# Kernel optimization log

Measured on AMD Instinct MI355X. Metric: run time of the kernel, lower is better.

The kernel has to match this reference:

```python
import jax, jax.numpy as jnp
import numpy as np

NUM_ROUTING = 3
EPS = 1e-8


def squash(s, axis):
    # s * (||s||^2 / (1 + ||s||^2)) / ||s||  along `axis`
    sq = jnp.sum(s * s, axis=axis, keepdims=True)
    return s * (sq / (1.0 + sq)) / jnp.sqrt(sq + EPS)


def setup_inputs() -> dict:
    key = jax.random.key(0)
    k1, k2 = jax.random.split(key)
    B, R, C, OUT, IN = 32, 2048, 32, 32, 16
    x = jax.random.normal(k1, (B, R, IN), dtype=jnp.float32)
    vote = jax.random.normal(k2, (R, C, OUT, IN), dtype=jnp.float32)
    return {"x": x, "vote": vote}


def reference(x, vote):
    # votes[b,r,c,o] = sum_i vote[r,c,o,i] * x[b,r,i]
    votes = jnp.einsum('rcoi,bri->brco', vote, x)  # [B,R,C,OUT]
    agreement = jnp.zeros_like(votes)
    verdict = None
    for _ in range(NUM_ROUTING):
        chairman = jax.nn.softmax(agreement, axis=1)          # softmax over routes
        summary = jnp.sum(chairman * votes, axis=1, keepdims=True)  # [B,1,C,OUT]
        verdict = squash(summary, axis=3)                     # squash over out_dim
        agreement = agreement + jnp.sum(votes * verdict, axis=3, keepdims=True)
    return verdict[:, 0, :, :]  # [B, C, OUT]
```

## Files before the change

### kernel.cpp

```cpp
#include <hip/hip_runtime.h>
#include <hip/hip_fp16.h>

#define B 32
#define R 2048
#define C 32
#define O 32
#define IN 16

typedef _Float16 hf2 __attribute__((ext_vector_type(2)));


__global__ __launch_bounds__(512, 4) void votes_kernel(
    const float* __restrict__ x,
    const float* __restrict__ vote,
    __half* __restrict__ votes_h)
{
  const int t = threadIdx.x;
  const int c = blockIdx.y * 2 + (t >> 8);
  const int tt = t & 255;
  const int rp_l = tt >> 4;
  const int op = tt & 15;
  const int r0 = blockIdx.x * 32;
  const int r = r0 + 2 * rp_l;
  const int rpg = blockIdx.x * 16 + rp_l;

  __shared__ unsigned int x_lds[32 * 32 * 8];

#pragma unroll
  for (int k = 0; k < 8; ++k) {
    int j = t + k * 512;
    int bb = j >> 7;
    int rr = (j >> 2) & 31;
    int ic = j & 3;
    float4 v = *reinterpret_cast<const float4*>(
        x + ((size_t)bb * R + r0 + rr) * IN + ic * 4);
    __half2 h01 = __float22half2_rn(make_float2(v.x, v.y));
    __half2 h23 = __float22half2_rn(make_float2(v.z, v.w));
    int w = (bb * 32 + rr) * 8 + 2 * ic;
    x_lds[w] = __builtin_bit_cast(unsigned int, h01);
    x_lds[w + 1] = __builtin_bit_cast(unsigned int, h23);
  }

  unsigned int wh[4][8];
#pragma unroll
  for (int p = 0; p < 2; ++p) {
#pragma unroll
    for (int q = 0; q < 2; ++q) {
      const float4* vp = reinterpret_cast<const float4*>(
          vote + (((size_t)(r + p) * C + c) * O + 2 * op + q) * IN);
#pragma unroll
      for (int k = 0; k < 4; ++k) {
        float4 f = vp[k];
        __half2 a = __float22half2_rn(make_float2(f.x, f.y));
        __half2 d = __float22half2_rn(make_float2(f.z, f.w));
        wh[p * 2 + q][2 * k] = __builtin_bit_cast(unsigned int, a);
        wh[p * 2 + q][2 * k + 1] = __builtin_bit_cast(unsigned int, d);
      }
    }
  }
  __syncthreads();

  __half* ob = votes_h + (size_t)c * 65536 + (size_t)rpg * 64 + op * 4;

#pragma unroll 2
  for (int bb = 0; bb < 32; ++bb) {
    const uint4* xr = reinterpret_cast<const uint4*>(
        &x_lds[(bb * 32 + 2 * rp_l) * 8]);
    uint4 xa = xr[0], xb = xr[1];
    uint4 xc = xr[2], xd = xr[3];
    unsigned int x0[8] = {xa.x, xa.y, xa.z, xa.w, xb.x, xb.y, xb.z, xb.w};
    unsigned int x1[8] = {xc.x, xc.y, xc.z, xc.w, xd.x, xd.y, xd.z, xd.w};
    float a00 = 0.f, a01 = 0.f, a10 = 0.f, a11 = 0.f;
#pragma unroll
    for (int k = 0; k < 8; ++k) {
      hf2 xv0 = __builtin_bit_cast(hf2, x0[k]);
      hf2 xv1 = __builtin_bit_cast(hf2, x1[k]);
      a00 = __builtin_amdgcn_fdot2(__builtin_bit_cast(hf2, wh[0][k]), xv0, a00, false);
      a01 = __builtin_amdgcn_fdot2(__builtin_bit_cast(hf2, wh[1][k]), xv0, a01, false);
      a10 = __builtin_amdgcn_fdot2(__builtin_bit_cast(hf2, wh[2][k]), xv1, a10, false);
      a11 = __builtin_amdgcn_fdot2(__builtin_bit_cast(hf2, wh[3][k]), xv1, a11, false);
    }
    __half2 w0 = __float22half2_rn(make_float2(a00, a10));
    __half2 w1 = __float22half2_rn(make_float2(a01, a11));
    uint2 pk;
    pk.x = __builtin_bit_cast(unsigned int, w0);
    pk.y = __builtin_bit_cast(unsigned int, w1);
    *reinterpret_cast<uint2*>(ob + (size_t)bb * C * 65536) = pk;
  }
}

__global__ __launch_bounds__(1024, 4) void routing_kernel(
    const __half* __restrict__ votes_h,
    float* __restrict__ out)
{
  const int b = blockIdx.x >> 5;
  const int c = blockIdx.x & 31;
  const int t = threadIdx.x;
  const int lane = t & 63;
  const int wave = t >> 6;
  const int g = t >> 5;
  const int o = t & 31;

  __shared__ unsigned int vmix[1024 * 34];
  __shared__ float2 e2[1024];
  __shared__ float red[32][33];
  __shared__ float vdf[32];
  __shared__ float scal_z[16];

  const uint4* src = reinterpret_cast<const uint4*>(
      votes_h + ((size_t)b * C + c) * 65536);
#pragma unroll
  for (int k = 0; k < 8; ++k) {
    int j = t + k * 1024;
    uint4 v = src[j];
    int rp = j >> 3;
    int q = j & 7;
    unsigned int* dst = &vmix[rp * 34 + 4 * q];
    uint2 a; a.x = v.x; a.y = v.y;
    uint2 d; d.x = v.z; d.y = v.w;
    *reinterpret_cast<uint2*>(dst) = a;
    *reinterpret_cast<uint2*>(dst + 2) = d;
  }
  __syncthreads();

  float a0 = 0.0f, a1 = 0.0f;
  float Zinv = 1.0f / 2048.0f;

  for (int iter = 0; iter < 3; ++iter) {
    if (iter > 0) {
      float e0 = __expf(a0), e1 = __expf(a1);
      float z = e0 + e1;
#pragma unroll
      for (int mask = 32; mask; mask >>= 1) z += __shfl_xor(z, mask);
      if (lane == 0) scal_z[wave] = z;
      e2[t] = make_float2(e0, e1);
      __syncthreads();
      float Z = 0.0f;
#pragma unroll
      for (int w = 0; w < 16; ++w) Z += scal_z[w];
      Zinv = 1.0f / Z;
    }

    {
      float s = 0.0f;
      const unsigned int* vb = &vmix[(size_t)g * 32 * 34 + o];
      if (iter == 0) {
#pragma unroll
        for (int j = 0; j < 32; ++j) {
          __half2 vv = __builtin_bit_cast(__half2, vb[j * 34]);
          s += __low2float(vv) + __high2float(vv);
        }
      } else {
        const float2* eb = &e2[g * 32];
#pragma unroll
        for (int j = 0; j < 32; ++j) {
          __half2 vv = __builtin_bit_cast(__half2, vb[j * 34]);
          float2 ee = eb[j];
          s += ee.x * __low2float(vv) + ee.y * __high2float(vv);
        }
      }
      red[o][g] = s;
    }
    __syncthreads();

    if (t < 32) {
      float S = 0.0f;
#pragma unroll
      for (int gg = 0; gg < 32; ++gg) S += red[t][gg];
      float summary = S * Zinv;
      float sq = summary * summary;
#pragma unroll
      for (int mask = 16; mask; mask >>= 1) sq += __shfl_xor(sq, mask);
      float scale = sq / ((1.0f + sq) * sqrtf(sq + 1e-8f));
      float vd = summary * scale;
      vdf[t] = vd;
      if (iter == 2) out[((size_t)b * C + c) * O + t] = vd;
    }
    __syncthreads();

    if (iter < 2) {
      float u0 = 0.0f, u1 = 0.0f;
      const unsigned int* vb = &vmix[(size_t)t * 34];
#pragma unroll
      for (int q = 0; q < 16; ++q) {
        uint2 vv = *reinterpret_cast<const uint2*>(vb + 2 * q);
        __half2 va = __builtin_bit_cast(__half2, vv.x);
        __half2 vbh = __builtin_bit_cast(__half2, vv.y);
        float vda = vdf[2 * q], vdb = vdf[2 * q + 1];
        u0 += __low2float(va) * vda + __low2float(vbh) * vdb;
        u1 += __high2float(va) * vda + __high2float(vbh) * vdb;
      }
      a0 += u0;
      a1 += u1;
    }
  }
}

extern "C" void kernel_launch(void* const* d_in, const int* in_sizes, int n_in,
                              void* d_out, int out_size, void* d_ws, size_t ws_size,
                              hipStream_t stream) {
  const float* x = (const float*)d_in[0];
  const float* vote = (const float*)d_in[1];
  float* out = (float*)d_out;
  __half* votes_h = (__half*)d_ws;

  votes_kernel<<<dim3(R / 32, C / 2), 512, 0, stream>>>(x, vote, votes_h);
  routing_kernel<<<dim3(B * C), 1024, 0, stream>>>(votes_h, out);
}
```

Before: 284.0 us.

## Split votes kernel over batch quarters and fuse first routing sum into load

The votes kernel now gives each block a single capsule c and 16 routes, with threads split across four batch quarters. This shrinks the shared x tile and raises the occupancy hint at the cost of reloading vote weights for more blocks. The routing kernel computes the iteration-0 uniform sum while staging votes into shared memory, using shuffle reductions, so the first strided shared-memory pass is skipped. An extra barrier is added at the end of each routing iteration.

```diff
diff --git a/kernel.cpp b/kernel.cpp
--- a/kernel.cpp
+++ b/kernel.cpp
@@ -10,33 +10,33 @@
 typedef _Float16 hf2 __attribute__((ext_vector_type(2)));
 
 
-__global__ __launch_bounds__(512, 4) void votes_kernel(
+__global__ __launch_bounds__(512, 6) void votes_kernel(
     const float* __restrict__ x,
     const float* __restrict__ vote,
     __half* __restrict__ votes_h)
 {
   const int t = threadIdx.x;
-  const int c = blockIdx.y * 2 + (t >> 8);
-  const int tt = t & 255;
-  const int rp_l = tt >> 4;
-  const int op = tt & 15;
-  const int r0 = blockIdx.x * 32;
+  const int c = blockIdx.y;
+  const int bq = t >> 7;
+  const int rp_l = (t >> 4) & 7;
+  const int op = t & 15;
+  const int r0 = blockIdx.x * 16;
   const int r = r0 + 2 * rp_l;
-  const int rpg = blockIdx.x * 16 + rp_l;
-
-  __shared__ unsigned int x_lds[32 * 32 * 8];
-
-#pragma unroll
-  for (int k = 0; k < 8; ++k) {
+  const int rpg = blockIdx.x * 8 + rp_l;
+
+  __shared__ unsigned int x_lds[32 * 16 * 8];
+
+#pragma unroll
+  for (int k = 0; k < 4; ++k) {
     int j = t + k * 512;
-    int bb = j >> 7;
-    int rr = (j >> 2) & 31;
+    int bb = j >> 6;
+    int rr = (j >> 2) & 15;
     int ic = j & 3;
     float4 v = *reinterpret_cast<const float4*>(
         x + ((size_t)bb * R + r0 + rr) * IN + ic * 4);
     __half2 h01 = __float22half2_rn(make_float2(v.x, v.y));
     __half2 h23 = __float22half2_rn(make_float2(v.z, v.w));
-    int w = (bb * 32 + rr) * 8 + 2 * ic;
+    int w = (bb * 16 + rr) * 8 + 2 * ic;
     x_lds[w] = __builtin_bit_cast(unsigned int, h01);
     x_lds[w + 1] = __builtin_bit_cast(unsigned int, h23);
   }
@@ -62,10 +62,11 @@
 
   __half* ob = votes_h + (size_t)c * 65536 + (size_t)rpg * 64 + op * 4;
 
-#pragma unroll 2
-  for (int bb = 0; bb < 32; ++bb) {
+#pragma unroll
+  for (int jj = 0; jj < 8; ++jj) {
+    const int bb = bq * 8 + jj;
     const uint4* xr = reinterpret_cast<const uint4*>(
-        &x_lds[(bb * 32 + 2 * rp_l) * 8]);
+        &x_lds[(bb * 16 + 2 * rp_l) * 8]);
     uint4 xa = xr[0], xb = xr[1];
     uint4 xc = xr[2], xd = xr[3];
     unsigned int x0[8] = {xa.x, xa.y, xa.z, xa.w, xb.x, xb.y, xb.z, xb.w};
@@ -104,30 +105,51 @@
   __shared__ unsigned int vmix[1024 * 34];
   __shared__ float2 e2[1024];
   __shared__ float red[32][33];
+  __shared__ float s0red[16][8][4];
   __shared__ float vdf[32];
   __shared__ float scal_z[16];
 
   const uint4* src = reinterpret_cast<const uint4*>(
       votes_h + ((size_t)b * C + c) * 65536);
+  const int o4 = t & 7;
+  float s4[4] = {0.f, 0.f, 0.f, 0.f};
 #pragma unroll
   for (int k = 0; k < 8; ++k) {
     int j = t + k * 1024;
     uint4 v = src[j];
     int rp = j >> 3;
-    int q = j & 7;
-    unsigned int* dst = &vmix[rp * 34 + 4 * q];
+    unsigned int* dst = &vmix[rp * 34 + 4 * o4];
     uint2 a; a.x = v.x; a.y = v.y;
     uint2 d; d.x = v.z; d.y = v.w;
     *reinterpret_cast<uint2*>(dst) = a;
     *reinterpret_cast<uint2*>(dst + 2) = d;
+    __half2 h0 = __builtin_bit_cast(__half2, v.x);
+    __half2 h1 = __builtin_bit_cast(__half2, v.y);
+    __half2 h2 = __builtin_bit_cast(__half2, v.z);
+    __half2 h3 = __builtin_bit_cast(__half2, v.w);
+    s4[0] += __low2float(h0) + __high2float(h0);
+    s4[1] += __low2float(h1) + __high2float(h1);
+    s4[2] += __low2float(h2) + __high2float(h2);
+    s4[3] += __low2float(h3) + __high2float(h3);
+  }
+#pragma unroll
+  for (int mask = 8; mask <= 32; mask <<= 1) {
+#pragma unroll
+    for (int m = 0; m < 4; ++m) s4[m] += __shfl_xor(s4[m], mask);
+  }
+  if (lane < 8) {
+#pragma unroll
+    for (int m = 0; m < 4; ++m) s0red[wave][lane][m] = s4[m];
   }
   __syncthreads();
 
   float a0 = 0.0f, a1 = 0.0f;
-  float Zinv = 1.0f / 2048.0f;
 
   for (int iter = 0; iter < 3; ++iter) {
-    if (iter > 0) {
+    float Zinv;
+    if (iter == 0) {
+      Zinv = 1.0f / 2048.0f;
+    } else {
       float e0 = __expf(a0), e1 = __expf(a1);
       float z = e0 + e1;
 #pragma unroll
@@ -139,34 +161,29 @@
 #pragma unroll
       for (int w = 0; w < 16; ++w) Z += scal_z[w];
       Zinv = 1.0f / Z;
-    }
-
-    {
+
       float s = 0.0f;
       const unsigned int* vb = &vmix[(size_t)g * 32 * 34 + o];
-      if (iter == 0) {
-#pragma unroll
-        for (int j = 0; j < 32; ++j) {
-          __half2 vv = __builtin_bit_cast(__half2, vb[j * 34]);
-          s += __low2float(vv) + __high2float(vv);
-        }
-      } else {
-        const float2* eb = &e2[g * 32];
-#pragma unroll
-        for (int j = 0; j < 32; ++j) {
-          __half2 vv = __builtin_bit_cast(__half2, vb[j * 34]);
-          float2 ee = eb[j];
-          s += ee.x * __low2float(vv) + ee.y * __high2float(vv);
-        }
+      const float2* eb = &e2[g * 32];
+#pragma unroll
+      for (int j = 0; j < 32; ++j) {
+        __half2 vv = __builtin_bit_cast(__half2, vb[j * 34]);
+        float2 ee = eb[j];
+        s += ee.x * __low2float(vv) + ee.y * __high2float(vv);
       }
       red[o][g] = s;
-    }
-    __syncthreads();
+      __syncthreads();
+    }
 
     if (t < 32) {
       float S = 0.0f;
-#pragma unroll
-      for (int gg = 0; gg < 32; ++gg) S += red[t][gg];
+      if (iter == 0) {
+#pragma unroll
+        for (int w = 0; w < 16; ++w) S += s0red[w][t >> 2][t & 3];
+      } else {
+#pragma unroll
+        for (int gg = 0; gg < 32; ++gg) S += red[t][gg];
+      }
       float summary = S * Zinv;
       float sq = summary * summary;
 #pragma unroll
@@ -192,6 +209,7 @@
       }
       a0 += u0;
       a1 += u1;
+      __syncthreads();
     }
   }
 }
@@ -204,6 +222,6 @@
   float* out = (float*)d_out;
   __half* votes_h = (__half*)d_ws;
 
-  votes_kernel<<<dim3(R / 32, C / 2), 512, 0, stream>>>(x, vote, votes_h);
+  votes_kernel<<<dim3(R / 16, C), 512, 0, stream>>>(x, vote, votes_h);
   routing_kernel<<<dim3(B * C), 1024, 0, stream>>>(votes_h, out);
 }
```

Result: slower. 299.0 us (+5.3%).
